# Optimization experiments

Hardware: AMD Instinct MI355X
Metric: run time of the kernel (lower is better)

The kernel has to match this reference:

```python
import jax, jax.numpy as jnp
import numpy as np

N_NODES = 50000
N_EDGES = 800000
IN_CH = 64
OC = 16  # out_channels


def setup_inputs() -> dict:
    key = jax.random.key(0)
    ks = jax.random.split(key, 16)
    x = jax.random.normal(ks[0], (N_NODES, IN_CH), dtype=jnp.float32)
    edge_index = jax.random.randint(ks[1], (2, N_EDGES), 0, N_NODES, dtype=jnp.int64)

    def lin(k, fan_in, fan_out):
        s = 1.0 / np.sqrt(fan_in)
        return jax.random.uniform(k, (fan_in, fan_out), jnp.float32, -s, s)

    d1, d2 = 16 * OC, 8 * OC  # 256, 128
    return {
        "x": x,
        "W1_rel": lin(ks[2], IN_CH, d1), "b1": jnp.zeros((d1,), jnp.float32), "W1_root": lin(ks[3], IN_CH, d1),
        "W2_rel": lin(ks[4], d1, d2), "b2": jnp.zeros((d2,), jnp.float32), "W2_root": lin(ks[5], d1, d2),
        "Wmu_rel": lin(ks[6], d2, OC), "bmu": jnp.zeros((OC,), jnp.float32), "Wmu_root": lin(ks[7], d2, OC),
        "Wls_rel": lin(ks[8], d2, OC), "bls": jnp.zeros((OC,), jnp.float32), "Wls_root": lin(ks[9], d2, OC),
        "edge_index": edge_index,
    }


def _graph_conv(x, src, dst, deg_inv, W_rel, b, W_root):
    # PyG GraphConv(aggr='mean'): out = lin_rel(mean_{j in N(i)} x_j) + lin_root(x_i)
    msg_sum = jax.ops.segment_sum(x[src], dst, num_segments=x.shape[0])  # [N, d]
    agg = msg_sum * deg_inv[:, None]
    return agg @ W_rel + b + x @ W_root


def reference(x, W1_rel, b1, W1_root, W2_rel, b2, W2_root,
              Wmu_rel, bmu, Wmu_root, Wls_rel, bls, Wls_root, edge_index):
    src, dst = edge_index[0], edge_index[1]
    deg = jax.ops.segment_sum(jnp.ones_like(dst, dtype=x.dtype), dst, num_segments=x.shape[0])
    deg_inv = jnp.where(deg > 0, 1.0 / jnp.maximum(deg, 1.0), 0.0)

    h = jax.nn.relu(_graph_conv(x, src, dst, deg_inv, W1_rel, b1, W1_root))
    h = jax.nn.relu(_graph_conv(h, src, dst, deg_inv, W2_rel, b2, W2_root))
    mu = _graph_conv(h, src, dst, deg_inv, Wmu_rel, bmu, Wmu_root)
    logstd = _graph_conv(h, src, dst, deg_inv, Wls_rel, bls, Wls_root)
    return (mu, logstd)
```

## Files before the change

kernel.cpp:

```cpp
#include <hip/hip_runtime.h>
#include <hip/hip_fp8.h>

#define N_NODES 50000
#define N_EDGES 800000
#define NBUCK 196
#define PBLK 391
#define CAP 5120

typedef unsigned short ushort_t;
typedef unsigned char uchar_t;
typedef short short8 __attribute__((ext_vector_type(8)));
typedef float floatx4 __attribute__((ext_vector_type(4)));

__device__ __forceinline__ float bf2f(ushort_t u) {
    unsigned v = ((unsigned)u) << 16;
    return __builtin_bit_cast(float, v);
}
__device__ __forceinline__ ushort_t f2bf(float f) {
    unsigned u = __builtin_bit_cast(unsigned, f);
    unsigned r = (u + 0x7FFFu + ((u >> 16) & 1u)) >> 16;
    return (ushort_t)r;
}
__device__ __forceinline__ uchar_t f2fp8(float f) {
    __hip_fp8_e4m3 t(f);
    return (uchar_t)t.__x;
}
__device__ __forceinline__ float fp82f(uchar_t u) {
    __hip_fp8_e4m3 t;
    t.__x = (__hip_fp8_storage_t)u;
    return (float)t;
}
__device__ __forceinline__ float4 ld4(const float* p) { return *(const float4*)p; }

__global__ __launch_bounds__(256) void prep_kernel(
    const float* __restrict__ x,
    const float* __restrict__ W1_rel, const float* __restrict__ W1_root,
    const float* __restrict__ W2_rel, const float* __restrict__ W2_root,
    const float* __restrict__ Wmu_rel, const float* __restrict__ Wls_rel,
    const float* __restrict__ Wmu_root, const float* __restrict__ Wls_root,
    ushort_t* __restrict__ ax, uchar_t* __restrict__ xq,
    ushort_t* __restrict__ B1t, ushort_t* __restrict__ B2t, ushort_t* __restrict__ B3t,
    int* __restrict__ bcursor) {
    int idx = blockIdx.x * blockDim.x + threadIdx.x;
    if (idx < 400000) {
        int n = idx >> 3, c = (idx & 7) * 8;
        float4 v0 = ld4(x + (size_t)n * 64 + c);
        float4 v1 = ld4(x + (size_t)n * 64 + c + 4);
        float vv[8] = {v0.x, v0.y, v0.z, v0.w, v1.x, v1.y, v1.z, v1.w};
        short8 o;
        unsigned q0 = 0, q1 = 0;
        #pragma unroll
        for (int i = 0; i < 4; ++i) {
            o[i] = f2bf(vv[i]);
            o[4 + i] = f2bf(vv[4 + i]);
            q0 |= ((unsigned)f2fp8(vv[i])) << (8 * i);
            q1 |= ((unsigned)f2fp8(vv[4 + i])) << (8 * i);
        }
        *(short8*)(ax + (size_t)n * 128 + 64 + c) = o;
        uint2 q = {q0, q1};
        *(uint2*)(xq + (size_t)n * 64 + c) = q;
    } else if (idx < 506496) {
        int j = idx - 400000;
        if (j < 32768) {
            int n = j >> 7, k = j & 127;
            float v = (k < 64) ? W1_rel[k * 256 + n] : W1_root[(k - 64) * 256 + n];
            B1t[j] = f2bf(v);
        } else if (j < 98304) {
            int jj = j - 32768;
            int n = jj >> 8, k = jj & 255;
            float v = (n < 128) ? W2_rel[k * 128 + n] : W2_root[k * 128 + (n - 128)];
            B2t[jj] = f2bf(v);
        } else {
            int jj = j - 98304;
            int n = jj >> 7, k = jj & 127;
            const float* W = (n < 16) ? Wmu_rel : (n < 32) ? Wls_rel : (n < 48) ? Wmu_root : Wls_root;
            B3t[jj] = f2bf(W[k * 16 + (n & 15)]);
        }
    } else if (idx < 506496 + NBUCK) {
        int b = idx - 506496;
        bcursor[b] = b * CAP;
    }
}

__global__ __launch_bounds__(256) void partition_kernel(
    const int* __restrict__ src, const int* __restrict__ dst,
    int* __restrict__ bcursor, unsigned* __restrict__ pairbuf) {
    __shared__ int h[NBUCK];
    __shared__ int cur[NBUCK];
    const int tid = threadIdx.x;
    for (int i = tid; i < NBUCK; i += 256) h[i] = 0;
    __syncthreads();
    const int base = blockIdx.x * 2048;
    int d[8];
    #pragma unroll
    for (int j = 0; j < 8; ++j) {
        int e = base + j * 256 + tid;
        if (e < N_EDGES) { d[j] = dst[e]; atomicAdd(&h[d[j] >> 8], 1); }
        else d[j] = -1;
    }
    __syncthreads();
    for (int i = tid; i < NBUCK; i += 256) {
        int c = h[i];
        cur[i] = c ? atomicAdd(&bcursor[i], c) : 0;
    }
    __syncthreads();
    #pragma unroll
    for (int j = 0; j < 8; ++j) {
        int e = base + j * 256 + tid;
        if (e < N_EDGES) {
            int dd = d[j];
            int slot = atomicAdd(&cur[dd >> 8], 1);
            pairbuf[slot] = (unsigned)src[e] | ((unsigned)(dd & 255) << 16);
        }
    }
}

__global__ __launch_bounds__(256) void fill_bucket_kernel(
    const unsigned* __restrict__ pairbuf, const int* __restrict__ bcursor,
    int* __restrict__ row_beg, int* __restrict__ row_end,
    float* __restrict__ dinv, ushort_t* __restrict__ eidx) {
    __shared__ int h[256];
    __shared__ int sm[256];
    __shared__ int cur[256];
    const int b = blockIdx.x, tid = threadIdx.x;
    const int beg = b * CAP, end = bcursor[b];
    h[tid] = 0;
    __syncthreads();
    for (int i = beg + tid; i < end; i += 256)
        atomicAdd(&h[pairbuf[i] >> 16], 1);
    __syncthreads();
    int c = h[tid];
    sm[tid] = c;
    __syncthreads();
    #pragma unroll
    for (int off = 1; off < 256; off <<= 1) {
        int t = (tid >= off) ? sm[tid - off] : 0;
        __syncthreads();
        sm[tid] += t;
        __syncthreads();
    }
    int exc = beg + sm[tid] - c;
    int node = b * 256 + tid;
    if (node < N_NODES) {
        row_beg[node] = exc;
        row_end[node] = exc + c;
        dinv[node] = c > 0 ? 1.0f / (float)c : 0.0f;
    }
    cur[tid] = exc;
    __syncthreads();
    for (int i = beg + tid; i < end; i += 256) {
        unsigned v = pairbuf[i];
        int slot = atomicAdd(&cur[v >> 16], 1);
        eidx[slot] = (ushort_t)(v & 0xFFFFu);
    }
}

__global__ __launch_bounds__(256) void gather1_kernel(
    const int* __restrict__ row_beg, const int* __restrict__ row_end,
    const ushort_t* __restrict__ eidx, const float* __restrict__ dinv,
    const uchar_t* __restrict__ xq, ushort_t* __restrict__ ax) {
    const int lane = threadIdx.x & 7;
    const int nl = threadIdx.x >> 3;
    const int n = blockIdx.x * 32 + nl;
    if (n >= N_NODES) return;
    const int beg = row_beg[n], end = row_end[n];
    float a0[8] = {}, a1[8] = {}, a2[8] = {}, a3[8] = {};
    int j = beg;
    for (; j + 3 < end; j += 4) {
        uint2 v0 = *(const uint2*)(xq + (size_t)eidx[j] * 64 + lane * 8);
        uint2 v1 = *(const uint2*)(xq + (size_t)eidx[j + 1] * 64 + lane * 8);
        uint2 v2 = *(const uint2*)(xq + (size_t)eidx[j + 2] * 64 + lane * 8);
        uint2 v3 = *(const uint2*)(xq + (size_t)eidx[j + 3] * 64 + lane * 8);
        #pragma unroll
        for (int i = 0; i < 4; ++i) {
            a0[i]     += fp82f((uchar_t)(v0.x >> (8 * i)));
            a0[4 + i] += fp82f((uchar_t)(v0.y >> (8 * i)));
            a1[i]     += fp82f((uchar_t)(v1.x >> (8 * i)));
            a1[4 + i] += fp82f((uchar_t)(v1.y >> (8 * i)));
            a2[i]     += fp82f((uchar_t)(v2.x >> (8 * i)));
            a2[4 + i] += fp82f((uchar_t)(v2.y >> (8 * i)));
            a3[i]     += fp82f((uchar_t)(v3.x >> (8 * i)));
            a3[4 + i] += fp82f((uchar_t)(v3.y >> (8 * i)));
        }
    }
    for (; j < end; ++j) {
        uint2 v0 = *(const uint2*)(xq + (size_t)eidx[j] * 64 + lane * 8);
        #pragma unroll
        for (int i = 0; i < 4; ++i) {
            a0[i]     += fp82f((uchar_t)(v0.x >> (8 * i)));
            a0[4 + i] += fp82f((uchar_t)(v0.y >> (8 * i)));
        }
    }
    float d = dinv[n];
    short8 o;
    #pragma unroll
    for (int i = 0; i < 8; ++i) o[i] = f2bf(((a0[i] + a1[i]) + (a2[i] + a3[i])) * d);
    *(short8*)(ax + (size_t)n * 128 + lane * 8) = o;
}

__global__ __launch_bounds__(256) void gemm1_mfma(
    const ushort_t* __restrict__ A, const ushort_t* __restrict__ Bt,
    const float* __restrict__ b1, ushort_t* __restrict__ h1) {
    constexpr int K = 128, KP = K + 8;
    __shared__ ushort_t Bs[64 * KP];
    const int tid = threadIdx.x;
    const int w = tid >> 6, lane = tid & 63;
    const int ln = lane & 15, quad = lane >> 4;
    const int rowbase = blockIdx.x * 64 + w * 16;
    int r = rowbase + ln; if (r > N_NODES - 1) r = N_NODES - 1;
    short8 a[4];
    #pragma unroll
    for (int s = 0; s < 4; ++s)
        a[s] = *(const short8*)(A + (size_t)r * K + s * 32 + quad * 8);
    const int r0 = rowbase + quad * 4;
    for (int ny = 0; ny < 4; ++ny) {
        __syncthreads();
        for (int i = tid; i < 64 * 16; i += 256) {
            int row = i >> 4, off = (i & 15) * 8;
            *(short8*)(Bs + row * KP + off) = *(const short8*)(Bt + (size_t)(ny * 64 + row) * K + off);
        }
        __syncthreads();
        floatx4 acc[4] = {};
        #pragma unroll
        for (int f = 0; f < 4; ++f) {
            const ushort_t* bp = Bs + (f * 16 + ln) * KP + quad * 8;
            #pragma unroll
            for (int s = 0; s < 4; ++s) {
                short8 b = *(const short8*)(bp + s * 32);
                acc[f] = __builtin_amdgcn_mfma_f32_16x16x32_bf16(a[s], b, acc[f], 0, 0, 0);
            }
        }
        #pragma unroll
        for (int f = 0; f < 4; ++f) {
            int n = ny * 64 + f * 16 + ln;
            float bias = b1[n];
            #pragma unroll
            for (int g = 0; g < 4; ++g) {
                int rr = r0 + g;
                if (rr >= N_NODES) continue;
                h1[(size_t)rr * 256 + n] = f2bf(fmaxf(acc[f][g] + bias, 0.0f));
            }
        }
    }
}

__global__ __launch_bounds__(256) void gemm2_mfma(
    const ushort_t* __restrict__ A, const ushort_t* __restrict__ Bt,
    uchar_t* __restrict__ t2, ushort_t* __restrict__ r2) {
    constexpr int K = 256, KP = K + 8;
    __shared__ ushort_t Bs[64 * KP];
    const int tid = threadIdx.x;
    const int w = tid >> 6, lane = tid & 63;
    const int ln = lane & 15, quad = lane >> 4;
    const int rowbase = blockIdx.x * 64 + w * 16;
    int r = rowbase + ln; if (r > N_NODES - 1) r = N_NODES - 1;
    short8 a[8];
    #pragma unroll
    for (int s = 0; s < 8; ++s)
        a[s] = *(const short8*)(A + (size_t)r * K + s * 32 + quad * 8);
    const int r0 = rowbase + quad * 4;
    for (int ny = 0; ny < 4; ++ny) {
        __syncthreads();
        for (int i = tid; i < 64 * 32; i += 256) {
            int row = i >> 5, off = (i & 31) * 8;
            *(short8*)(Bs + row * KP + off) = *(const short8*)(Bt + (size_t)(ny * 64 + row) * K + off);
        }
        __syncthreads();
        floatx4 acc[4] = {};
        #pragma unroll
        for (int f = 0; f < 4; ++f) {
            const ushort_t* bp = Bs + (f * 16 + ln) * KP + quad * 8;
            #pragma unroll
            for (int s = 0; s < 8; ++s) {
                short8 b = *(const short8*)(bp + s * 32);
                acc[f] = __builtin_amdgcn_mfma_f32_16x16x32_bf16(a[s], b, acc[f], 0, 0, 0);
            }
        }
        #pragma unroll
        for (int f = 0; f < 4; ++f) {
            int n = ny * 64 + f * 16 + ln;
            #pragma unroll
            for (int g = 0; g < 4; ++g) {
                int rr = r0 + g;
                if (rr >= N_NODES) continue;
                float v = acc[f][g];
                if (n < 128) t2[(size_t)rr * 128 + n] = f2fp8(v);
                else r2[(size_t)rr * 128 + (n - 128)] = f2bf(v);
            }
        }
    }
}

__global__ __launch_bounds__(256) void g2g3_kernel(
    const uchar_t* __restrict__ t2, const ushort_t* __restrict__ r2,
    const int* __restrict__ row_beg, const int* __restrict__ row_end,
    const ushort_t* __restrict__ eidx, const float* __restrict__ dinv,
    const float* __restrict__ b2, const ushort_t* __restrict__ B3t,
    ushort_t* __restrict__ tml, float* __restrict__ rml) {
    constexpr int KP = 136;
    __shared__ ushort_t As[16 * KP];
    const int tid = threadIdx.x;
    const int nb = blockIdx.x * 16;
    {
        const int nl = tid >> 4, lane = tid & 15;
        const int node = nb + nl;
        const int beg = row_beg[node], end = row_end[node];
        float a0[8] = {}, a1[8] = {}, a2[8] = {}, a3[8] = {};
        int j = beg;
        for (; j + 3 < end; j += 4) {
            uint2 v0 = *(const uint2*)(t2 + (size_t)eidx[j] * 128 + lane * 8);
            uint2 v1 = *(const uint2*)(t2 + (size_t)eidx[j + 1] * 128 + lane * 8);
            uint2 v2 = *(const uint2*)(t2 + (size_t)eidx[j + 2] * 128 + lane * 8);
            uint2 v3 = *(const uint2*)(t2 + (size_t)eidx[j + 3] * 128 + lane * 8);
            #pragma unroll
            for (int i = 0; i < 4; ++i) {
                a0[i]     += fp82f((uchar_t)(v0.x >> (8 * i)));
                a0[4 + i] += fp82f((uchar_t)(v0.y >> (8 * i)));
                a1[i]     += fp82f((uchar_t)(v1.x >> (8 * i)));
                a1[4 + i] += fp82f((uchar_t)(v1.y >> (8 * i)));
                a2[i]     += fp82f((uchar_t)(v2.x >> (8 * i)));
                a2[4 + i] += fp82f((uchar_t)(v2.y >> (8 * i)));
                a3[i]     += fp82f((uchar_t)(v3.x >> (8 * i)));
                a3[4 + i] += fp82f((uchar_t)(v3.y >> (8 * i)));
            }
        }
        for (; j < end; ++j) {
            uint2 v0 = *(const uint2*)(t2 + (size_t)eidx[j] * 128 + lane * 8);
            #pragma unroll
            for (int i = 0; i < 4; ++i) {
                a0[i]     += fp82f((uchar_t)(v0.x >> (8 * i)));
                a0[4 + i] += fp82f((uchar_t)(v0.y >> (8 * i)));
            }
        }
        float d = dinv[node];
        short8 rv = *(const short8*)(r2 + (size_t)node * 128 + lane * 8);
        float4 ba = ld4(b2 + lane * 8), bb = ld4(b2 + lane * 8 + 4);
        float bc[8] = {ba.x, ba.y, ba.z, ba.w, bb.x, bb.y, bb.z, bb.w};
        short8 o;
        #pragma unroll
        for (int i = 0; i < 8; ++i)
            o[i] = f2bf(fmaxf(((a0[i] + a1[i]) + (a2[i] + a3[i])) * d + bf2f((ushort_t)rv[i]) + bc[i], 0.0f));
        *(short8*)(As + nl * KP + lane * 8) = o;
    }
    __syncthreads();
    const int w = tid >> 6, lane64 = tid & 63;
    const int ln = lane64 & 15, quad = lane64 >> 4;
    short8 a[4];
    #pragma unroll
    for (int s = 0; s < 4; ++s)
        a[s] = *(const short8*)(As + ln * KP + s * 32 + quad * 8);
    floatx4 acc = {};
    const ushort_t* bp = B3t + (size_t)(w * 16 + ln) * 128 + quad * 8;
    #pragma unroll
    for (int s = 0; s < 4; ++s) {
        short8 b = *(const short8*)(bp + s * 32);
        acc = __builtin_amdgcn_mfma_f32_16x16x32_bf16(a[s], b, acc, 0, 0, 0);
    }
    const int r0 = nb + quad * 4;
    const int ncol = w * 16 + ln;
    #pragma unroll
    for (int g = 0; g < 4; ++g) {
        int rr = r0 + g;
        float v = acc[g];
        if (ncol < 32) tml[(size_t)rr * 32 + ncol] = f2bf(v);
        else rml[(size_t)rr * 32 + (ncol - 32)] = v;
    }
}

__global__ __launch_bounds__(256) void gather3_kernel(
    const ushort_t* __restrict__ tml, const float* __restrict__ rml,
    const int* __restrict__ row_beg, const int* __restrict__ row_end,
    const ushort_t* __restrict__ eidx, const float* __restrict__ dinv,
    const float* __restrict__ bmu, const float* __restrict__ bls,
    float* __restrict__ out) {
    const int lane = threadIdx.x & 3;
    const int nl = threadIdx.x >> 2;
    const int n = blockIdx.x * 64 + nl;
    if (n >= N_NODES) return;
    const int beg = row_beg[n], end = row_end[n];
    float a0[8] = {}, a1[8] = {};
    int j = beg;
    for (; j + 1 < end; j += 2) {
        int s0 = eidx[j], s1 = eidx[j + 1];
        short8 v0 = *(const short8*)(tml + (size_t)s0 * 32 + lane * 8);
        short8 v1 = *(const short8*)(tml + (size_t)s1 * 32 + lane * 8);
        #pragma unroll
        for (int i = 0; i < 8; ++i) { a0[i] += bf2f((ushort_t)v0[i]); a1[i] += bf2f((ushort_t)v1[i]); }
    }
    if (j < end) {
        int s0 = eidx[j];
        short8 v0 = *(const short8*)(tml + (size_t)s0 * 32 + lane * 8);
        #pragma unroll
        for (int i = 0; i < 8; ++i) a0[i] += bf2f((ushort_t)v0[i]);
    }
    float d = dinv[n];
    const float* bias = (lane < 2) ? (bmu + lane * 8) : (bls + (lane - 2) * 8);
    float4 ra = ld4(rml + (size_t)n * 32 + lane * 8);
    float4 rb = ld4(rml + (size_t)n * 32 + lane * 8 + 4);
    float4 ba = ld4(bias);
    float4 bb = ld4(bias + 4);
    float rr[8] = {ra.x, ra.y, ra.z, ra.w, rb.x, rb.y, rb.z, rb.w};
    float bc[8] = {ba.x, ba.y, ba.z, ba.w, bb.x, bb.y, bb.z, bb.w};
    float res[8];
    #pragma unroll
    for (int i = 0; i < 8; ++i) res[i] = (a0[i] + a1[i]) * d + rr[i] + bc[i];
    float* base = (lane < 2) ? (out + (size_t)n * 16 + lane * 8)
                             : (out + 800000u + (size_t)n * 16 + (lane - 2) * 8);
    *(float4*)(base) = make_float4(res[0], res[1], res[2], res[3]);
    *(float4*)(base + 4) = make_float4(res[4], res[5], res[6], res[7]);
}

extern "C" void kernel_launch(void* const* d_in, const int* in_sizes, int n_in,
                              void* d_out, int out_size, void* d_ws, size_t ws_size,
                              hipStream_t stream) {
    const float* x       = (const float*)d_in[0];
    const float* W1_rel  = (const float*)d_in[1];
    const float* b1      = (const float*)d_in[2];
    const float* W1_root = (const float*)d_in[3];
    const float* W2_rel  = (const float*)d_in[4];
    const float* b2      = (const float*)d_in[5];
    const float* W2_root = (const float*)d_in[6];
    const float* Wmu_rel = (const float*)d_in[7];
    const float* bmu     = (const float*)d_in[8];
    const float* Wmu_root= (const float*)d_in[9];
    const float* Wls_rel = (const float*)d_in[10];
    const float* bls     = (const float*)d_in[11];
    const float* Wls_root= (const float*)d_in[12];
    const int*   ei      = (const int*)d_in[13];
    const int* src = ei;
    const int* dst = ei + N_EDGES;

    int*      bcursor = (int*)d_ws;
    int*      row_beg = bcursor + 256;
    int*      row_end = row_beg + 50048;
    unsigned* pairbuf = (unsigned*)(row_end + 50048);
    ushort_t* eidx    = (ushort_t*)(pairbuf + 1003520);
    float*    dinv    = (float*)(eidx + 1003520);
    ushort_t* ax   = (ushort_t*)(dinv + 50000);
    ushort_t* h1   = ax + 6400000;
    uchar_t*  t2   = (uchar_t*)(h1 + 12800000);
    uchar_t*  xq   = t2 + 6400000;
    ushort_t* r2   = (ushort_t*)(xq + 3200000);
    ushort_t* tml  = r2 + 6400000;
    ushort_t* B1t  = tml + 1600000;
    ushort_t* B2t  = B1t + 32768;
    ushort_t* B3t  = B2t + 65536;
    float* rml     = (float*)(B3t + 8192);
    float* out     = (float*)d_out;

    prep_kernel<<<1980, 256, 0, stream>>>(x, W1_rel, W1_root, W2_rel, W2_root,
                                          Wmu_rel, Wls_rel, Wmu_root, Wls_root,
                                          ax, xq, B1t, B2t, B3t, bcursor);
    partition_kernel<<<PBLK, 256, 0, stream>>>(src, dst, bcursor, pairbuf);
    fill_bucket_kernel<<<NBUCK, 256, 0, stream>>>(pairbuf, bcursor, row_beg, row_end, dinv, eidx);

    gather1_kernel<<<1563, 256, 0, stream>>>(row_beg, row_end, eidx, dinv, xq, ax);
    gemm1_mfma<<<782, 256, 0, stream>>>(ax, B1t, b1, h1);

    gemm2_mfma<<<782, 256, 0, stream>>>(h1, B2t, t2, r2);
    g2g3_kernel<<<3125, 256, 0, stream>>>(t2, r2, row_beg, row_end, eidx, dinv, b2, B3t, tml, rml);

    gather3_kernel<<<782, 256, 0, stream>>>(tml, rml, row_beg, row_end, eidx, dinv, bmu, bls, out);
}
```

Baseline: 221.1 us.

## Fuse layer-1 and layer-2 GEMMs, keeping h1 tile in shared memory

Merges the two MFMA GEMM kernels into one. Each block computes its 64-row tile of h1 (relu of ax·W1 plus bias) into LDS, then multiplies it by the layer-2 weights directly. This avoids writing and re-reading the bf16 h1 buffer (about 25.6 MB) through global memory and saves one launch. In exchange the kernel uses more LDS (about 52 KB per block), which may lower occupancy, and the second GEMM now loads its weights in smaller 32-column chunks with more barriers.

```diff
diff --git a/kernel.cpp b/kernel.cpp
--- a/kernel.cpp
+++ b/kernel.cpp
@@ -198,87 +198,79 @@
     *(short8*)(ax + (size_t)n * 128 + lane * 8) = o;
 }
 
-__global__ __launch_bounds__(256) void gemm1_mfma(
-    const ushort_t* __restrict__ A, const ushort_t* __restrict__ Bt,
-    const float* __restrict__ b1, ushort_t* __restrict__ h1) {
-    constexpr int K = 128, KP = K + 8;
-    __shared__ ushort_t Bs[64 * KP];
+__global__ __launch_bounds__(256) void g12_kernel(
+    const ushort_t* __restrict__ ax, const ushort_t* __restrict__ B1t,
+    const ushort_t* __restrict__ B2t, const float* __restrict__ b1,
+    uchar_t* __restrict__ t2, ushort_t* __restrict__ r2) {
+    constexpr int HP = 268;
+    __shared__ ushort_t H[64 * HP];
+    __shared__ ushort_t Bs[8704];
     const int tid = threadIdx.x;
     const int w = tid >> 6, lane = tid & 63;
     const int ln = lane & 15, quad = lane >> 4;
     const int rowbase = blockIdx.x * 64 + w * 16;
     int r = rowbase + ln; if (r > N_NODES - 1) r = N_NODES - 1;
-    short8 a[4];
-    #pragma unroll
-    for (int s = 0; s < 4; ++s)
-        a[s] = *(const short8*)(A + (size_t)r * K + s * 32 + quad * 8);
     const int r0 = rowbase + quad * 4;
-    for (int ny = 0; ny < 4; ++ny) {
+
+    {
+        short8 a1[4];
+        #pragma unroll
+        for (int s = 0; s < 4; ++s)
+            a1[s] = *(const short8*)(ax + (size_t)r * 128 + s * 32 + quad * 8);
+        for (int ny = 0; ny < 4; ++ny) {
+            __syncthreads();
+            for (int i = tid; i < 64 * 16; i += 256) {
+                int row = i >> 4, off = (i & 15) * 8;
+                *(short8*)(Bs + row * 136 + off) =
+                    *(const short8*)(B1t + (size_t)(ny * 64 + row) * 128 + off);
+            }
+            __syncthreads();
+            floatx4 acc[4] = {};
+            #pragma unroll
+            for (int f = 0; f < 4; ++f) {
+                const ushort_t* bp = Bs + (f * 16 + ln) * 136 + quad * 8;
+                #pragma unroll
+                for (int s = 0; s < 4; ++s) {
+                    short8 b = *(const short8*)(bp + s * 32);
+                    acc[f] = __builtin_amdgcn_mfma_f32_16x16x32_bf16(a1[s], b, acc[f], 0, 0, 0);
+                }
+            }
+            #pragma unroll
+            for (int f = 0; f < 4; ++f) {
+                int n = ny * 64 + f * 16 + ln;
+                float bias = b1[n];
+                #pragma unroll
+                for (int g = 0; g < 4; ++g)
+                    H[(w * 16 + quad * 4 + g) * HP + n] = f2bf(fmaxf(acc[f][g] + bias, 0.0f));
+            }
+        }
+    }
+    __syncthreads();
+    short8 a2[8];
+    #pragma unroll
+    for (int s = 0; s < 8; ++s)
+        a2[s] = *(const short8*)(H + (w * 16 + ln) * HP + s * 32 + quad * 8);
+    for (int t = 0; t < 8; ++t) {
+        if (t) __syncthreads();
+        for (int i = tid; i < 32 * 32; i += 256) {
+            int row = i >> 5, off = (i & 31) * 8;
+            *(short8*)(Bs + row * 264 + off) =
+                *(const short8*)(B2t + (size_t)(t * 32 + row) * 256 + off);
+        }
         __syncthreads();
-        for (int i = tid; i < 64 * 16; i += 256) {
-            int row = i >> 4, off = (i & 15) * 8;
-            *(short8*)(Bs + row * KP + off) = *(const short8*)(Bt + (size_t)(ny * 64 + row) * K + off);
-        }
-        __syncthreads();
-        floatx4 acc[4] = {};
-        #pragma unroll
-        for (int f = 0; f < 4; ++f) {
-            const ushort_t* bp = Bs + (f * 16 + ln) * KP + quad * 8;
-            #pragma unroll
-            for (int s = 0; s < 4; ++s) {
-                short8 b = *(const short8*)(bp + s * 32);
-                acc[f] = __builtin_amdgcn_mfma_f32_16x16x32_bf16(a[s], b, acc[f], 0, 0, 0);
-            }
-        }
-        #pragma unroll
-        for (int f = 0; f < 4; ++f) {
-            int n = ny * 64 + f * 16 + ln;
-            float bias = b1[n];
-            #pragma unroll
-            for (int g = 0; g < 4; ++g) {
-                int rr = r0 + g;
-                if (rr >= N_NODES) continue;
-                h1[(size_t)rr * 256 + n] = f2bf(fmaxf(acc[f][g] + bias, 0.0f));
-            }
-        }
-    }
-}
-
-__global__ __launch_bounds__(256) void gemm2_mfma(
-    const ushort_t* __restrict__ A, const ushort_t* __restrict__ Bt,
-    uchar_t* __restrict__ t2, ushort_t* __restrict__ r2) {
-    constexpr int K = 256, KP = K + 8;
-    __shared__ ushort_t Bs[64 * KP];
-    const int tid = threadIdx.x;
-    const int w = tid >> 6, lane = tid & 63;
-    const int ln = lane & 15, quad = lane >> 4;
-    const int rowbase = blockIdx.x * 64 + w * 16;
-    int r = rowbase + ln; if (r > N_NODES - 1) r = N_NODES - 1;
-    short8 a[8];
-    #pragma unroll
-    for (int s = 0; s < 8; ++s)
-        a[s] = *(const short8*)(A + (size_t)r * K + s * 32 + quad * 8);
-    const int r0 = rowbase + quad * 4;
-    for (int ny = 0; ny < 4; ++ny) {
-        __syncthreads();
-        for (int i = tid; i < 64 * 32; i += 256) {
-            int row = i >> 5, off = (i & 31) * 8;
-            *(short8*)(Bs + row * KP + off) = *(const short8*)(Bt + (size_t)(ny * 64 + row) * K + off);
-        }
-        __syncthreads();
-        floatx4 acc[4] = {};
-        #pragma unroll
-        for (int f = 0; f < 4; ++f) {
-            const ushort_t* bp = Bs + (f * 16 + ln) * KP + quad * 8;
+        floatx4 acc[2] = {};
+        #pragma unroll
+        for (int f = 0; f < 2; ++f) {
+            const ushort_t* bp = Bs + (f * 16 + ln) * 264 + quad * 8;
             #pragma unroll
             for (int s = 0; s < 8; ++s) {
                 short8 b = *(const short8*)(bp + s * 32);
-                acc[f] = __builtin_amdgcn_mfma_f32_16x16x32_bf16(a[s], b, acc[f], 0, 0, 0);
-            }
-        }
-        #pragma unroll
-        for (int f = 0; f < 4; ++f) {
-            int n = ny * 64 + f * 16 + ln;
+                acc[f] = __builtin_amdgcn_mfma_f32_16x16x32_bf16(a2[s], b, acc[f], 0, 0, 0);
+            }
+        }
+        #pragma unroll
+        for (int f = 0; f < 2; ++f) {
+            int n = t * 32 + f * 16 + ln;
             #pragma unroll
             for (int g = 0; g < 4; ++g) {
                 int rr = r0 + g;
@@ -437,8 +429,7 @@
     ushort_t* eidx    = (ushort_t*)(pairbuf + 1003520);
     float*    dinv    = (float*)(eidx + 1003520);
     ushort_t* ax   = (ushort_t*)(dinv + 50000);
-    ushort_t* h1   = ax + 6400000;
-    uchar_t*  t2   = (uchar_t*)(h1 + 12800000);
+    uchar_t*  t2   = (uchar_t*)(ax + 6400000);
     uchar_t*  xq   = t2 + 6400000;
     ushort_t* r2   = (ushort_t*)(xq + 3200000);
     ushort_t* tml  = r2 + 6400000;
@@ -455,9 +446,8 @@
     fill_bucket_kernel<<<NBUCK, 256, 0, stream>>>(pairbuf, bcursor, row_beg, row_end, dinv, eidx);
 
     gather1_kernel<<<1563, 256, 0, stream>>>(row_beg, row_end, eidx, dinv, xq, ax);
-    gemm1_mfma<<<782, 256, 0, stream>>>(ax, B1t, b1, h1);
-
-    gemm2_mfma<<<782, 256, 0, stream>>>(h1, B2t, t2, r2);
+    g12_kernel<<<782, 256, 0, stream>>>(ax, B1t, B2t, b1, t2, r2);
+
     g2g3_kernel<<<3125, 256, 0, stream>>>(t2, r2, row_beg, row_end, eidx, dinv, b2, B3t, tml, rml);
 
     gather3_kernel<<<782, 256, 0, stream>>>(tml, rml, row_beg, row_end, eidx, dinv, bmu, bls, out);
```

New measurement: 222.5 us. No clear change (+0.6%).
